# Performance work log

Hardware: AMD Instinct MI355X
Metric: run time of the kernel (lower is better)

Reference implementation:

```python
import jax, jax.numpy as jnp
import numpy as np

N_NODES = 400000
D_IN = 256
HIDDEN = 256
BATCH = 1024


def setup_inputs() -> dict:
    key = jax.random.key(0)
    k1, k2, k3, k4 = jax.random.split(key, 4)
    x = jax.random.normal(k1, (N_NODES, D_IN), dtype=jnp.float32)
    graph_idx = jnp.sort(jax.random.randint(k2, (N_NODES,), 0, BATCH)).astype(jnp.int64)
    # Linear(-1, hidden) params
    W = jax.random.normal(k3, (HIDDEN, D_IN), dtype=jnp.float32) / np.sqrt(D_IN)
    b = jnp.zeros((HIDDEN,), dtype=jnp.float32)
    # SoftmaxAggregation learnable per-channel temperature, PyG init = 1.0
    t = jnp.ones((1, HIDDEN), dtype=jnp.float32)
    return {"x": x, "graph_idx": graph_idx, "batch_size": BATCH, "W": W, "b": b, "t": t}


def _segment_softmax(a, idx, num_segments):
    # per-segment, per-channel numerically-stable softmax (PyG softmax)
    m = jax.ops.segment_max(a, idx, num_segments=num_segments)  # [B, C]
    e = jnp.exp(a - m[idx])
    s = jax.ops.segment_sum(e, idx, num_segments=num_segments)  # [B, C]
    return e / (s[idx] + 1e-16)


def reference(x, graph_idx, batch_size, W, b, t):
    idx = graph_idx.astype(jnp.int32)
    h = jax.nn.relu(x @ W.T + b)                      # [N, C]
    alpha = _segment_softmax(h * t, idx, batch_size)  # [N, C]
    agg = jax.ops.segment_sum(h * alpha, idx, num_segments=batch_size)  # [B, C]
    # graph_tran = MLP(n_graph_trans=0, ...) is identity
    return agg.reshape(batch_size, -1)
```

## Files before the change

### kernel.cpp

```cpp
#include <hip/hip_runtime.h>
#include <hip/hip_bf16.h>


typedef __attribute__((ext_vector_type(8))) short short8;
typedef __attribute__((ext_vector_type(4))) float f32x4;
typedef __attribute__((ext_vector_type(4))) unsigned u32x4;
typedef __attribute__((ext_vector_type(2))) unsigned u32x2;

#define D_INN 256
#define HID 256
#define BM 64
#define NGRID 256
#define NTHREADS 512
#define PSB 544

__device__ __forceinline__ unsigned pk2(float a, float b) {
    unsigned r;
    asm("v_cvt_pk_bf16_f32 %0, %1, %2" : "=v"(r) : "v"(a), "v"(b));
    return r;
}

__global__ void zero_sp(float* __restrict__ sp) {
    int i = blockIdx.x * blockDim.x + threadIdx.x;
    ((f32x4*)sp)[i] = (f32x4){0.f, 0.f, 0.f, 0.f};
}

__global__ void finalize(const float* __restrict__ S, const float* __restrict__ P,
                         float* __restrict__ out) {
    int i = blockIdx.x * blockDim.x + threadIdx.x;
    out[i] = P[i] / (S[i] + 1e-16f);
}

template<int MODE>
__global__ __launch_bounds__(NTHREADS, 2) void gemm_fused(
    const float* __restrict__ x, const int* __restrict__ gidx,
    const float* __restrict__ W, const float* __restrict__ bias,
    const float* __restrict__ temp, float* __restrict__ part, float* __restrict__ P,
    int NT)
{
    __shared__ __align__(16) short Alds[2][BM * (PSB / 2)];
    __shared__ uint4 Mlds[32];

    const int t = threadIdx.x;
    const int w = t >> 6;
    const int l = t & 63;
    const int lrow = l & 15;
    const int lq = l >> 4;
    const int blk = blockIdx.x;

#pragma unroll
    for (int k = 0; k < 4; ++k) {
        const int it = w + k * 8;
        const int tile = blk + it * NGRID;
        if (tile < NT) {
            const int sid = gidx[(size_t)tile * BM + l];
            const int s0 = __shfl(sid, 0);
            const int s63 = __shfl(sid, 63);
            const unsigned long long m = __ballot(sid != s0);
            if (l == 0)
                Mlds[it] = make_uint4((unsigned)s0, (unsigned)s63,
                                      (unsigned)m, (unsigned)(m >> 32));
        }
    }

    short8 bvAll[2][8];
#pragma unroll
    for (int ni = 0; ni < 2; ++ni)
#pragma unroll
        for (int ks = 0; ks < 8; ++ks) {
            const float* wp = W + (size_t)(w * 32 + ni * 16 + lrow) * D_INN + ks * 32 + lq * 8;
            float4 a = ((const float4*)wp)[0];
            float4 b = ((const float4*)wp)[1];
            u32x4 ua;
            ua.x = pk2(a.x, a.y); ua.y = pk2(a.z, a.w);
            ua.z = pk2(b.x, b.y); ua.w = pk2(b.z, b.w);
            bvAll[ni][ks] = __builtin_bit_cast(short8, ua);
        }
    float bb[2], tt[2];
#pragma unroll
    for (int ni = 0; ni < 2; ++ni) {
        bb[ni] = bias[w * 32 + ni * 16 + lrow];
        tt[ni] = temp[w * 32 + ni * 16 + lrow];
    }

    char* const wr0 = (char*)&Alds[0][0] + (w * PSB) + l * 8;
    char* const wr1 = (char*)&Alds[1][0] + (w * PSB) + l * 8;
    const int rb = lrow * PSB + lq * 16;

    float4 ra[8], rbuf[8];

#define LOAD8(dst, tile)                                                        \
    {                                                                           \
        const float4* xp = (const float4*)(x + (size_t)(tile) * (BM * D_INN)) + t; \
        _Pragma("unroll")                                                       \
        for (int r = 0; r < 8; ++r) dst[r] = xp[r * 512];                       \
    }

#define CVTW(src, wrbase)                                                       \
    {                                                                           \
        _Pragma("unroll")                                                       \
        for (int r = 0; r < 8; ++r) {                                           \
            u32x2 p;                                                            \
            p.x = pk2(src[r].x, src[r].y);                                      \
            p.y = pk2(src[r].z, src[r].w);                                      \
            *(u32x2*)(wrbase + r * 8 * PSB) = p;                                \
        }                                                                       \
    }

#define COMPUTE_STORE(bufidx, it, jt)                                           \
    {                                                                           \
        const uint4 mt = Mlds[it];                                              \
        f32x4 acc[4][2];                                                        \
        _Pragma("unroll")                                                       \
        for (int i = 0; i < 4; ++i)                                             \
            _Pragma("unroll")                                                   \
            for (int j = 0; j < 2; ++j) acc[i][j] = (f32x4){0.f, 0.f, 0.f, 0.f};\
        const char* lb = (const char*)&Alds[bufidx][0] + rb;                    \
        _Pragma("unroll")                                                       \
        for (int ks = 0; ks < 8; ++ks) {                                        \
            short8 av[4];                                                       \
            _Pragma("unroll")                                                   \
            for (int mi = 0; mi < 4; ++mi)                                      \
                av[mi] = *(const short8*)(lb + mi * 16 * PSB + ks * 64);        \
            _Pragma("unroll")                                                   \
            for (int mi = 0; mi < 4; ++mi)                                      \
                _Pragma("unroll")                                               \
                for (int ni = 0; ni < 2; ++ni)                                  \
                    acc[mi][ni] = __builtin_amdgcn_mfma_f32_16x16x32_bf16(      \
                        av[mi], bvAll[ni][ks], acc[mi][ni], 0, 0, 0);           \
        }                                                                       \
        const int s0 = (int)mt.x, s63 = (int)mt.y;                              \
        float* pb = part + ((size_t)(jt) << 10);                                \
        int himask = 0;                                                         \
        _Pragma("unroll")                                                       \
        for (int mi = 0; mi < 4; ++mi) {                                        \
            const unsigned mk = (mi < 2) ? mt.z : mt.w;                         \
            const int base = (mi & 1) * 16 + lq * 4;                            \
            _Pragma("unroll")                                                   \
            for (int j = 0; j < 4; ++j)                                         \
                if ((mk >> (base + j)) & 1) himask |= 1 << (mi * 4 + j);        \
        }                                                                       \
        _Pragma("unroll")                                                       \
        for (int ni = 0; ni < 2; ++ni) {                                        \
            float es0 = 0.f, ps0 = 0.f, es1 = 0.f, ps1 = 0.f;                   \
            _Pragma("unroll")                                                   \
            for (int mi = 0; mi < 4; ++mi)                                      \
                _Pragma("unroll")                                               \
                for (int j = 0; j < 4; ++j) {                                   \
                    float h = fmaxf(acc[mi][ni][j] + bb[ni], 0.f);              \
                    float e = __expf(h * tt[ni]);                               \
                    if ((himask >> (mi * 4 + j)) & 1) { es1 += e; ps1 += h * e; }\
                    else                              { es0 += e; ps0 += h * e; }\
                }                                                               \
            es0 += __shfl_xor(es0, 16); ps0 += __shfl_xor(ps0, 16);             \
            es0 += __shfl_xor(es0, 32); ps0 += __shfl_xor(ps0, 32);             \
            es1 += __shfl_xor(es1, 16); ps1 += __shfl_xor(ps1, 16);             \
            es1 += __shfl_xor(es1, 32); ps1 += __shfl_xor(ps1, 32);             \
            if (l < 16) {                                                       \
                const int ch = w * 32 + ni * 16 + lrow;                         \
                if (MODE == 1) {                                                \
                    atomicAdd(&part[(size_t)s0 * HID + ch], es0);               \
                    atomicAdd(&P[(size_t)s0 * HID + ch], ps0);                  \
                    atomicAdd(&part[(size_t)s63 * HID + ch], es1);              \
                    atomicAdd(&P[(size_t)s63 * HID + ch], ps1);                 \
                } else {                                                        \
                    f32x4 v; v.x = es0; v.y = ps0; v.z = es1; v.w = ps1;        \
                    *(f32x4*)&pb[4 * ch] = v;                                   \
                }                                                               \
            }                                                                   \
        }                                                                       \
    }

#define FENCE_BARRIER()                                          \
    asm volatile("s_waitcnt lgkmcnt(0)" ::: "memory");           \
    __builtin_amdgcn_s_barrier();                                \
    __builtin_amdgcn_sched_barrier(0);

    LOAD8(ra, blk);
    LOAD8(rbuf, blk + NGRID);
    __builtin_amdgcn_sched_barrier(0);
    CVTW(ra, wr0);
    FENCE_BARRIER();

    for (int it = 0;; it += 2) {
        {
            const int n = blk + it * NGRID;
            if (n >= NT) break;
            const int tgt = n + 2 * NGRID;
            if (tgt < NT) LOAD8(ra, tgt);
            __builtin_amdgcn_sched_barrier(0);
            COMPUTE_STORE(0, it, n);
            if (n + NGRID < NT) {
                CVTW(rbuf, wr1);
                FENCE_BARRIER();
            }
        }
        {
            const int n = blk + (it + 1) * NGRID;
            if (n >= NT) break;
            const int tgt = n + 2 * NGRID;
            if (tgt < NT) LOAD8(rbuf, tgt);
            __builtin_amdgcn_sched_barrier(0);
            COMPUTE_STORE(1, it + 1, n);
            if (n + NGRID < NT) {
                CVTW(ra, wr0);
                FENCE_BARRIER();
            }
        }
    }
#undef LOAD8
#undef CVTW
#undef COMPUTE_STORE
#undef FENCE_BARRIER
}

__global__ void reduce_seg(const int* __restrict__ gidx, const float* __restrict__ part,
                           float* __restrict__ out, int N) {
    const int g = blockIdx.x;
    const int ch = threadIdx.x;
    int lo = 0, hi = N;
    while (lo < hi) { int m = (lo + hi) >> 1; if (gidx[m] < g) lo = m + 1; else hi = m; }
    const int r0 = lo;
    hi = N;
    while (lo < hi) { int m = (lo + hi) >> 1; if (gidx[m] < g + 1) lo = m + 1; else hi = m; }
    const int r1 = lo;
    float es = 0.f, ps = 0.f;
    if (r0 < r1) {
        const int b0 = r0 >> 6, b1 = (r1 - 1) >> 6;
        for (int b = b0; b <= b1; ++b) {
            const f32x4* pb = (const f32x4*)(part + ((size_t)b << 10));
            f32x4 v = pb[ch];
            if (gidx[b << 6] == g) { es += v.x; ps += v.y; }
            else                   { es += v.z; ps += v.w; }
        }
    }
    out[(size_t)g * HID + ch] = ps / (es + 1e-16f);
}

extern "C" void kernel_launch(void* const* d_in, const int* in_sizes, int n_in,
                              void* d_out, int out_size, void* d_ws, size_t ws_size,
                              hipStream_t stream) {
    const float* x    = (const float*)d_in[0];
    const int*   gidx = (const int*)d_in[1];
    const float* W    = (const float*)d_in[3];
    const float* bias = (const float*)d_in[4];
    const float* temp = (const float*)d_in[5];
    float* out = (float*)d_out;

    const int N = in_sizes[1];
    const int B = out_size / HID;
    const int NT = N / BM;

    const size_t partFloats = (size_t)NT * 1024;
    const size_t need = partFloats * 4;

    if (ws_size >= need) {
        float* part = (float*)d_ws;
        gemm_fused<0><<<NGRID, NTHREADS, 0, stream>>>(x, gidx, W, bias, temp, part, nullptr, NT);
        reduce_seg<<<B, 256, 0, stream>>>(gidx, part, out, N);
    } else {
        float* S = (float*)d_ws;
        float* P = S + (size_t)B * HID;
        zero_sp<<<(2 * B * HID) / (256 * 4), 256, 0, stream>>>(S);
        gemm_fused<1><<<NGRID, NTHREADS, 0, stream>>>(x, gidx, W, bias, temp, S, P, NT);
        finalize<<<(B * HID) / 256, 256, 0, stream>>>(S, P, out);
    }
}
```

Measured before the change: 120.0 us.

## Software-pipeline epilogue of previous tile with MFMA loop of current tile

New measurement: 148.3 us. 1.24x slower.

```diff
diff --git a/kernel.cpp b/kernel.cpp
--- a/kernel.cpp
+++ b/kernel.cpp
@@ -88,6 +88,7 @@
     const int rb = lrow * PSB + lq * 16;
 
     float4 ra[8], rbuf[8];
+    f32x4 accE[4][2], accO[4][2];
 
 #define LOAD8(dst, tile)                                                        \
     {                                                                           \
@@ -107,14 +108,12 @@
         }                                                                       \
     }
 
-#define COMPUTE_STORE(bufidx, it, jt)                                           \
-    {                                                                           \
-        const uint4 mt = Mlds[it];                                              \
-        f32x4 acc[4][2];                                                        \
+#define KLOOP(bufidx, accv)                                                     \
+    {                                                                           \
         _Pragma("unroll")                                                       \
         for (int i = 0; i < 4; ++i)                                             \
             _Pragma("unroll")                                                   \
-            for (int j = 0; j < 2; ++j) acc[i][j] = (f32x4){0.f, 0.f, 0.f, 0.f};\
+            for (int j = 0; j < 2; ++j) accv[i][j] = (f32x4){0.f, 0.f, 0.f, 0.f};\
         const char* lb = (const char*)&Alds[bufidx][0] + rb;                    \
         _Pragma("unroll")                                                       \
         for (int ks = 0; ks < 8; ++ks) {                                        \
@@ -126,11 +125,16 @@
             for (int mi = 0; mi < 4; ++mi)                                      \
                 _Pragma("unroll")                                               \
                 for (int ni = 0; ni < 2; ++ni)                                  \
-                    acc[mi][ni] = __builtin_amdgcn_mfma_f32_16x16x32_bf16(      \
-                        av[mi], bvAll[ni][ks], acc[mi][ni], 0, 0, 0);           \
-        }                                                                       \
+                    accv[mi][ni] = __builtin_amdgcn_mfma_f32_16x16x32_bf16(     \
+                        av[mi], bvAll[ni][ks], accv[mi][ni], 0, 0, 0);          \
+        }                                                                       \
+    }
+
+#define EPILOGUE(accv, itv, jtv)                                                \
+    {                                                                           \
+        const uint4 mt = Mlds[itv];                                             \
         const int s0 = (int)mt.x, s63 = (int)mt.y;                              \
-        float* pb = part + ((size_t)(jt) << 10);                                \
+        float* pb = part + ((size_t)(jtv) << 10);                               \
         int himask = 0;                                                         \
         _Pragma("unroll")                                                       \
         for (int mi = 0; mi < 4; ++mi) {                                        \
@@ -147,7 +151,7 @@
             for (int mi = 0; mi < 4; ++mi)                                      \
                 _Pragma("unroll")                                               \
                 for (int j = 0; j < 4; ++j) {                                   \
-                    float h = fmaxf(acc[mi][ni][j] + bb[ni], 0.f);              \
+                    float h = fmaxf(accv[mi][ni][j] + bb[ni], 0.f);             \
                     float e = __expf(h * tt[ni]);                               \
                     if ((himask >> (mi * 4 + j)) & 1) { es1 += e; ps1 += h * e; }\
                     else                              { es0 += e; ps0 += h * e; }\
@@ -182,35 +186,55 @@
     CVTW(ra, wr0);
     FENCE_BARRIER();
 
-    for (int it = 0;; it += 2) {
+    {
+        LOAD8(ra, blk + 2 * NGRID);
+        __builtin_amdgcn_sched_barrier(0);
+        KLOOP(0, accE);
+        if (blk + NGRID < NT) {
+            CVTW(rbuf, wr1);
+            FENCE_BARRIER();
+        }
+    }
+
+    for (int it = 1;; it += 2) {
         {
             const int n = blk + it * NGRID;
             if (n >= NT) break;
             const int tgt = n + 2 * NGRID;
-            if (tgt < NT) LOAD8(ra, tgt);
-            __builtin_amdgcn_sched_barrier(0);
-            COMPUTE_STORE(0, it, n);
-            if (n + NGRID < NT) {
-                CVTW(rbuf, wr1);
-                FENCE_BARRIER();
-            }
-        }
-        {
-            const int n = blk + (it + 1) * NGRID;
-            if (n >= NT) break;
-            const int tgt = n + 2 * NGRID;
             if (tgt < NT) LOAD8(rbuf, tgt);
             __builtin_amdgcn_sched_barrier(0);
-            COMPUTE_STORE(1, it + 1, n);
+            EPILOGUE(accE, it - 1, n - NGRID);
+            KLOOP(1, accO);
             if (n + NGRID < NT) {
                 CVTW(ra, wr0);
                 FENCE_BARRIER();
             }
         }
+        {
+            const int n2 = blk + (it + 1) * NGRID;
+            if (n2 >= NT) break;
+            const int tgt2 = n2 + 2 * NGRID;
+            if (tgt2 < NT) LOAD8(ra, tgt2);
+            __builtin_amdgcn_sched_barrier(0);
+            EPILOGUE(accO, it, n2 - NGRID);
+            KLOOP(0, accE);
+            if (n2 + NGRID < NT) {
+                CVTW(rbuf, wr1);
+                FENCE_BARRIER();
+            }
+        }
+    }
+
+    {
+        const int lastIt = (NT - 1 - blk) / NGRID;
+        const int lastJt = blk + lastIt * NGRID;
+        if (lastIt & 1) { EPILOGUE(accO, lastIt, lastJt); }
+        else            { EPILOGUE(accE, lastIt, lastJt); }
     }
 #undef LOAD8
 #undef CVTW
-#undef COMPUTE_STORE
+#undef KLOOP
+#undef EPILOGUE
 #undef FENCE_BARRIER
 }
 
```

## Deepen LDS pipeline to four buffers, two tiles per barrier

Applied to the files above, without the earlier changes.

Result: slower. 135.2 us (+12.7%).

```diff
diff --git a/kernel.cpp b/kernel.cpp
--- a/kernel.cpp
+++ b/kernel.cpp
@@ -13,6 +13,7 @@
 #define NGRID 256
 #define NTHREADS 512
 #define PSB 544
+#define BUFSH (BM * (PSB / 2))
 
 __device__ __forceinline__ unsigned pk2(float a, float b) {
     unsigned r;
@@ -38,7 +39,7 @@
     const float* __restrict__ temp, float* __restrict__ part, float* __restrict__ P,
     int NT)
 {
-    __shared__ __align__(16) short Alds[2][BM * (PSB / 2)];
+    __shared__ __align__(16) short Alds[4][BUFSH];
     __shared__ uint4 Mlds[32];
 
     const int t = threadIdx.x;
@@ -83,8 +84,7 @@
         tt[ni] = temp[w * 32 + ni * 16 + lrow];
     }
 
-    char* const wr0 = (char*)&Alds[0][0] + (w * PSB) + l * 8;
-    char* const wr1 = (char*)&Alds[1][0] + (w * PSB) + l * 8;
+    const int wroff = w * PSB + l * 8;
     const int rb = lrow * PSB + lq * 16;
 
     float4 ra[8], rbuf[8];
@@ -96,8 +96,9 @@
         for (int r = 0; r < 8; ++r) dst[r] = xp[r * 512];                       \
     }
 
-#define CVTW(src, wrbase)                                                       \
-    {                                                                           \
+#define CVTW(src, bufi)                                                         \
+    {                                                                           \
+        char* wrbase = (char*)&Alds[bufi][0] + wroff;                           \
         _Pragma("unroll")                                                       \
         for (int r = 0; r < 8; ++r) {                                           \
             u32x2 p;                                                            \
@@ -176,42 +177,45 @@
     __builtin_amdgcn_s_barrier();                                \
     __builtin_amdgcn_sched_barrier(0);
 
+#define BODY(SV, BA, BB, BC, BD)                                                \
+    {                                                                           \
+        const int n0 = blk + (2 * (SV)) * NGRID;                                \
+        if (n0 >= NT) goto done;                                                \
+        const int n1 = n0 + NGRID;                                              \
+        if (n1 < NT) {                                                          \
+            if (n0 + 2 * NGRID < NT) { CVTW(ra, BC); }                          \
+            if (n1 + 2 * NGRID < NT) { CVTW(rbuf, BD); }                        \
+            if (n0 + 4 * NGRID < NT) { LOAD8(ra, n0 + 4 * NGRID); }             \
+            if (n1 + 4 * NGRID < NT) { LOAD8(rbuf, n1 + 4 * NGRID); }           \
+            __builtin_amdgcn_sched_barrier(0);                                  \
+            COMPUTE_STORE(BA, 2 * (SV), n0);                                    \
+            COMPUTE_STORE(BB, 2 * (SV) + 1, n1);                                \
+            if (n0 + 2 * NGRID < NT) { FENCE_BARRIER(); }                       \
+        } else {                                                                \
+            COMPUTE_STORE(BA, 2 * (SV), n0);                                    \
+            goto done;                                                          \
+        }                                                                       \
+    }
+
     LOAD8(ra, blk);
     LOAD8(rbuf, blk + NGRID);
     __builtin_amdgcn_sched_barrier(0);
-    CVTW(ra, wr0);
+    CVTW(ra, 0);
+    CVTW(rbuf, 1);
+    LOAD8(ra, blk + 2 * NGRID);
+    LOAD8(rbuf, blk + 3 * NGRID);
     FENCE_BARRIER();
 
-    for (int it = 0;; it += 2) {
-        {
-            const int n = blk + it * NGRID;
-            if (n >= NT) break;
-            const int tgt = n + 2 * NGRID;
-            if (tgt < NT) LOAD8(ra, tgt);
-            __builtin_amdgcn_sched_barrier(0);
-            COMPUTE_STORE(0, it, n);
-            if (n + NGRID < NT) {
-                CVTW(rbuf, wr1);
-                FENCE_BARRIER();
-            }
-        }
-        {
-            const int n = blk + (it + 1) * NGRID;
-            if (n >= NT) break;
-            const int tgt = n + 2 * NGRID;
-            if (tgt < NT) LOAD8(rbuf, tgt);
-            __builtin_amdgcn_sched_barrier(0);
-            COMPUTE_STORE(1, it + 1, n);
-            if (n + NGRID < NT) {
-                CVTW(ra, wr0);
-                FENCE_BARRIER();
-            }
-        }
-    }
+    for (int s = 0;; s += 2) {
+        BODY(s, 0, 1, 2, 3);
+        BODY(s + 1, 2, 3, 0, 1);
+    }
+done: ;
 #undef LOAD8
 #undef CVTW
 #undef COMPUTE_STORE
 #undef FENCE_BARRIER
+#undef BODY
 }
 
 __global__ void reduce_seg(const int* __restrict__ gidx, const float* __restrict__ part,
```

## Double row tile to 128 nodes and restructure prefetch pipeline in halves

Applied to the files above, without the earlier changes.

After: 129.9 us. 8.2% more time.

```diff
diff --git a/kernel.cpp b/kernel.cpp
--- a/kernel.cpp
+++ b/kernel.cpp
@@ -9,10 +9,11 @@
 
 #define D_INN 256
 #define HID 256
-#define BM 64
+#define BM 128
 #define NGRID 256
 #define NTHREADS 512
 #define PSB 544
+#define BUFSH (BM * (PSB / 2))
 
 __device__ __forceinline__ unsigned pk2(float a, float b) {
     unsigned r;
@@ -38,8 +39,8 @@
     const float* __restrict__ temp, float* __restrict__ part, float* __restrict__ P,
     int NT)
 {
-    __shared__ __align__(16) short Alds[2][BM * (PSB / 2)];
-    __shared__ uint4 Mlds[32];
+    __shared__ __align__(16) short Alds[2][BUFSH];
+    __shared__ uint4 Mlds[16][2];
 
     const int t = threadIdx.x;
     const int w = t >> 6;
@@ -49,17 +50,21 @@
     const int blk = blockIdx.x;
 
 #pragma unroll
-    for (int k = 0; k < 4; ++k) {
+    for (int k = 0; k < 2; ++k) {
         const int it = w + k * 8;
         const int tile = blk + it * NGRID;
         if (tile < NT) {
-            const int sid = gidx[(size_t)tile * BM + l];
-            const int s0 = __shfl(sid, 0);
-            const int s63 = __shfl(sid, 63);
-            const unsigned long long m = __ballot(sid != s0);
-            if (l == 0)
-                Mlds[it] = make_uint4((unsigned)s0, (unsigned)s63,
-                                      (unsigned)m, (unsigned)(m >> 32));
+            const int sidA = gidx[(size_t)tile * BM + l];
+            const int sidB = gidx[(size_t)tile * BM + 64 + l];
+            const int s0 = __shfl(sidA, 0);
+            const int sL = __shfl(sidB, 63);
+            const unsigned long long mA = __ballot(sidA != s0);
+            const unsigned long long mB = __ballot(sidB != s0);
+            if (l == 0) {
+                Mlds[it][0] = make_uint4((unsigned)s0, (unsigned)sL,
+                                         (unsigned)mA, (unsigned)(mA >> 32));
+                Mlds[it][1] = make_uint4((unsigned)mB, (unsigned)(mB >> 32), 0u, 0u);
+            }
         }
     }
 
@@ -83,21 +88,22 @@
         tt[ni] = temp[w * 32 + ni * 16 + lrow];
     }
 
-    char* const wr0 = (char*)&Alds[0][0] + (w * PSB) + l * 8;
-    char* const wr1 = (char*)&Alds[1][0] + (w * PSB) + l * 8;
+    const int wroff = w * PSB + l * 8;
     const int rb = lrow * PSB + lq * 16;
 
     float4 ra[8], rbuf[8];
 
-#define LOAD8(dst, tile)                                                        \
+#define LOAD8H(dst, tile, half)                                                 \
     {                                                                           \
-        const float4* xp = (const float4*)(x + (size_t)(tile) * (BM * D_INN)) + t; \
+        const float4* xp = (const float4*)(x + (size_t)(tile) * (BM * D_INN)    \
+                                             + (half) * 64 * D_INN) + t;        \
         _Pragma("unroll")                                                       \
         for (int r = 0; r < 8; ++r) dst[r] = xp[r * 512];                       \
     }
 
-#define CVTW(src, wrbase)                                                       \
+#define CVTW(src, bufi, half)                                                   \
     {                                                                           \
+        char* wrbase = (char*)&Alds[bufi][0] + (half) * 64 * PSB + wroff;       \
         _Pragma("unroll")                                                       \
         for (int r = 0; r < 8; ++r) {                                           \
             u32x2 p;                                                            \
@@ -109,42 +115,44 @@
 
 #define COMPUTE_STORE(bufidx, it, jt)                                           \
     {                                                                           \
-        const uint4 mt = Mlds[it];                                              \
-        f32x4 acc[4][2];                                                        \
-        _Pragma("unroll")                                                       \
-        for (int i = 0; i < 4; ++i)                                             \
+        const uint4 mt0 = Mlds[it][0];                                          \
+        const uint4 mt1 = Mlds[it][1];                                          \
+        f32x4 acc[8][2];                                                        \
+        _Pragma("unroll")                                                       \
+        for (int i = 0; i < 8; ++i)                                             \
             _Pragma("unroll")                                                   \
             for (int j = 0; j < 2; ++j) acc[i][j] = (f32x4){0.f, 0.f, 0.f, 0.f};\
         const char* lb = (const char*)&Alds[bufidx][0] + rb;                    \
         _Pragma("unroll")                                                       \
         for (int ks = 0; ks < 8; ++ks) {                                        \
-            short8 av[4];                                                       \
-            _Pragma("unroll")                                                   \
-            for (int mi = 0; mi < 4; ++mi)                                      \
+            short8 av[8];                                                       \
+            _Pragma("unroll")                                                   \
+            for (int mi = 0; mi < 8; ++mi)                                      \
                 av[mi] = *(const short8*)(lb + mi * 16 * PSB + ks * 64);        \
             _Pragma("unroll")                                                   \
-            for (int mi = 0; mi < 4; ++mi)                                      \
+            for (int mi = 0; mi < 8; ++mi)                                      \
                 _Pragma("unroll")                                               \
                 for (int ni = 0; ni < 2; ++ni)                                  \
                     acc[mi][ni] = __builtin_amdgcn_mfma_f32_16x16x32_bf16(      \
                         av[mi], bvAll[ni][ks], acc[mi][ni], 0, 0, 0);           \
         }                                                                       \
-        const int s0 = (int)mt.x, s63 = (int)mt.y;                              \
+        const int s0 = (int)mt0.x, sL = (int)mt0.y;                             \
         float* pb = part + ((size_t)(jt) << 10);                                \
-        int himask = 0;                                                         \
-        _Pragma("unroll")                                                       \
-        for (int mi = 0; mi < 4; ++mi) {                                        \
-            const unsigned mk = (mi < 2) ? mt.z : mt.w;                         \
+        unsigned himask = 0;                                                    \
+        _Pragma("unroll")                                                       \
+        for (int mi = 0; mi < 8; ++mi) {                                        \
+            const unsigned mk = (mi < 2) ? mt0.z : (mi < 4) ? mt0.w             \
+                              : (mi < 6) ? mt1.x : mt1.y;                       \
             const int base = (mi & 1) * 16 + lq * 4;                            \
             _Pragma("unroll")                                                   \
             for (int j = 0; j < 4; ++j)                                         \
-                if ((mk >> (base + j)) & 1) himask |= 1 << (mi * 4 + j);        \
+                if ((mk >> (base + j)) & 1) himask |= 1u << (mi * 4 + j);       \
         }                                                                       \
         _Pragma("unroll")                                                       \
         for (int ni = 0; ni < 2; ++ni) {                                        \
             float es0 = 0.f, ps0 = 0.f, es1 = 0.f, ps1 = 0.f;                   \
             _Pragma("unroll")                                                   \
-            for (int mi = 0; mi < 4; ++mi)                                      \
+            for (int mi = 0; mi < 8; ++mi)                                      \
                 _Pragma("unroll")                                               \
                 for (int j = 0; j < 4; ++j) {                                   \
                     float h = fmaxf(acc[mi][ni][j] + bb[ni], 0.f);              \
@@ -161,8 +169,8 @@
                 if (MODE == 1) {                                                \
                     atomicAdd(&part[(size_t)s0 * HID + ch], es0);               \
                     atomicAdd(&P[(size_t)s0 * HID + ch], ps0);                  \
-                    atomicAdd(&part[(size_t)s63 * HID + ch], es1);              \
-                    atomicAdd(&P[(size_t)s63 * HID + ch], ps1);                 \
+                    atomicAdd(&part[(size_t)sL * HID + ch], es1);               \
+                    atomicAdd(&P[(size_t)sL * HID + ch], ps1);                  \
                 } else {                                                        \
                     f32x4 v; v.x = es0; v.y = ps0; v.z = es1; v.w = ps1;        \
                     *(f32x4*)&pb[4 * ch] = v;                                   \
@@ -176,39 +184,30 @@
     __builtin_amdgcn_s_barrier();                                \
     __builtin_amdgcn_sched_barrier(0);
 
-    LOAD8(ra, blk);
-    LOAD8(rbuf, blk + NGRID);
+    LOAD8H(ra, blk, 0);
+    LOAD8H(rbuf, blk, 1);
     __builtin_amdgcn_sched_barrier(0);
-    CVTW(ra, wr0);
+    CVTW(ra, 0, 0);
+    CVTW(rbuf, 0, 1);
+    LOAD8H(rbuf, blk + NGRID, 0);
     FENCE_BARRIER();
 
-    for (int it = 0;; it += 2) {
-        {
-            const int n = blk + it * NGRID;
-            if (n >= NT) break;
-            const int tgt = n + 2 * NGRID;
-            if (tgt < NT) LOAD8(ra, tgt);
-            __builtin_amdgcn_sched_barrier(0);
-            COMPUTE_STORE(0, it, n);
-            if (n + NGRID < NT) {
-                CVTW(rbuf, wr1);
-                FENCE_BARRIER();
-            }
-        }
-        {
-            const int n = blk + (it + 1) * NGRID;
-            if (n >= NT) break;
-            const int tgt = n + 2 * NGRID;
-            if (tgt < NT) LOAD8(rbuf, tgt);
-            __builtin_amdgcn_sched_barrier(0);
-            COMPUTE_STORE(1, it + 1, n);
-            if (n + NGRID < NT) {
-                CVTW(ra, wr0);
-                FENCE_BARRIER();
-            }
-        }
-    }
-#undef LOAD8
+    for (int it = 0;; ++it) {
+        const int jt = blk + it * NGRID;
+        if (jt >= NT) break;
+        const int nxt = jt + NGRID;
+        const bool more = nxt < NT;
+        if (more) { LOAD8H(ra, nxt, 1); }
+        __builtin_amdgcn_sched_barrier(0);
+        COMPUTE_STORE(it & 1, it, jt);
+        if (more) {
+            CVTW(rbuf, (it + 1) & 1, 0);
+            CVTW(ra, (it + 1) & 1, 1);
+            if (nxt + NGRID < NT) { LOAD8H(rbuf, nxt + NGRID, 0); }
+            FENCE_BARRIER();
+        }
+    }
+#undef LOAD8H
 #undef CVTW
 #undef COMPUTE_STORE
 #undef FENCE_BARRIER
@@ -226,11 +225,11 @@
     const int r1 = lo;
     float es = 0.f, ps = 0.f;
     if (r0 < r1) {
-        const int b0 = r0 >> 6, b1 = (r1 - 1) >> 6;
+        const int b0 = r0 >> 7, b1 = (r1 - 1) >> 7;
         for (int b = b0; b <= b1; ++b) {
             const f32x4* pb = (const f32x4*)(part + ((size_t)b << 10));
             f32x4 v = pb[ch];
-            if (gidx[b << 6] == g) { es += v.x; ps += v.y; }
+            if (gidx[b << 7] == g) { es += v.x; ps += v.y; }
             else                   { es += v.z; ps += v.w; }
         }
     }
```
